# Performance work log

Measured on AMD Instinct MI355X. Metric: run time of the kernel, lower is better.

## Reference

```python
import jax, jax.numpy as jnp
import numpy as np

ACT_BIT = 8
W_BIT = 8
EPS = 1e-8


def ste_round(x):
    # straight-through round (matches torch STE quant autograd)
    return x + jax.lax.stop_gradient(jnp.round(x) - x)


def quant_act(x):
    """Per-tensor symmetric 8-bit activation quantization (HAWQ QuantAct)."""
    n = 2 ** (ACT_BIT - 1) - 1  # 127
    x_max = jax.lax.stop_gradient(jnp.max(jnp.abs(x)))
    scale = jnp.maximum(x_max, EPS) / n
    x_int = jnp.clip(ste_round(x / scale), -n - 1, n)
    return x_int * scale, scale


def quant_linear(x_q, act_scale, weight, bias):
    """Per-channel symmetric 8-bit weight quant + integer matmul + fused dequant."""
    n = 2 ** (W_BIT - 1) - 1  # 127
    w_max = jax.lax.stop_gradient(jnp.max(jnp.abs(weight), axis=1, keepdims=True))  # [out,1]
    w_scale = jnp.maximum(w_max, EPS) / n                                            # [out,1]
    w_int = jnp.clip(ste_round(weight / w_scale), -n - 1, n)                         # [out,in]
    bias_scale = w_scale[:, 0] * act_scale                                           # [out]
    b_int = ste_round(bias / bias_scale)                                             # [out]
    x_int = x_q / act_scale                                   # integer-valued float, [..., in]
    out_int = jnp.einsum('...i,oi->...o', x_int, w_int)       # int8-domain GEMM in float
    return (out_int + b_int) * bias_scale                     # fused dequant


def setup_inputs() -> dict:
    key = jax.random.key(0)
    k1, k2, k3 = jax.random.split(key, 3)
    L, B, Q, D, O = 6, 8, 1024, 1024, 1024
    hs = jax.random.normal(k1, (L, B, Q, D), dtype=jnp.float32)
    weight = jax.random.normal(k2, (O, D), dtype=jnp.float32) * 0.02
    bias = jax.random.normal(k3, (O,), dtype=jnp.float32) * 0.02
    return {"hs": hs, "weight": weight, "bias": bias}


def reference(hs, weight, bias):
    x_q, act_scale = quant_act(hs)
    return quant_linear(x_q, act_scale, weight, bias)
```

## Files before the change

kernel.cpp:

```cpp
#include <hip/hip_runtime.h>
#include <stdint.h>

typedef int i32x4 __attribute__((ext_vector_type(4)));

#define K_DIM 1024
#define BM 256
#define BN 256
#define BKK 64
#define NKT (K_DIM / BKK)


__device__ __forceinline__ int quant1(float v, float inv) {
  float t = rintf(v * inv);
  t = fminf(fmaxf(t, -128.0f), 127.0f);
  return (int)t;
}

__device__ __forceinline__ void gld_lds16(const signed char* g, signed char* l) {
  typedef const __attribute__((address_space(1))) unsigned int* gp_t;
  typedef __attribute__((address_space(3))) unsigned int* lp_t;
  __builtin_amdgcn_global_load_lds((gp_t)(const void*)g, (lp_t)(void*)l, 16, 0, 0);
}

__global__ void absmax_kernel(const float* __restrict__ x, unsigned int* __restrict__ amax,
                              long long n4) {
  long long i = (long long)blockIdx.x * blockDim.x + threadIdx.x;
  const long long stride = (long long)gridDim.x * blockDim.x;
  const float4* x4 = (const float4*)x;
  float m = 0.0f;
  for (; i < n4; i += stride) {
    float4 v = x4[i];
    m = fmaxf(m, fmaxf(fmaxf(fabsf(v.x), fabsf(v.y)), fmaxf(fabsf(v.z), fabsf(v.w))));
  }
#pragma unroll
  for (int off = 32; off > 0; off >>= 1) m = fmaxf(m, __shfl_down(m, off, 64));
  __shared__ float sm[4];
  const int lane = threadIdx.x & 63, wid = threadIdx.x >> 6;
  if (lane == 0) sm[wid] = m;
  __syncthreads();
  if (threadIdx.x == 0) {
    float b = fmaxf(fmaxf(sm[0], sm[1]), fmaxf(sm[2], sm[3]));
    atomicMax(amax, __float_as_uint(b));
  }
}

__global__ void wquant_kernel(const float* __restrict__ w, const float* __restrict__ bias,
                              const unsigned int* __restrict__ amax_u,
                              signed char* __restrict__ wq,
                              float* __restrict__ bscale, float* __restrict__ bint) {
  const int o = blockIdx.x;
  const int t = threadIdx.x;
  float4 v = ((const float4*)(w + (size_t)o * K_DIM))[t];
  float m = fmaxf(fmaxf(fabsf(v.x), fabsf(v.y)), fmaxf(fabsf(v.z), fabsf(v.w)));
#pragma unroll
  for (int off = 32; off > 0; off >>= 1) m = fmaxf(m, __shfl_down(m, off, 64));
  __shared__ float sm[4];
  __shared__ float s_scale;
  const int lane = t & 63, wid = t >> 6;
  if (lane == 0) sm[wid] = m;
  __syncthreads();
  if (t == 0) {
    float wm = fmaxf(fmaxf(sm[0], sm[1]), fmaxf(sm[2], sm[3]));
    float wsc = fmaxf(wm, 1e-8f) / 127.0f;
    float asc = fmaxf(__uint_as_float(*amax_u), 1e-8f) / 127.0f;
    float bsc = wsc * asc;
    bscale[o] = bsc;
    bint[o] = rintf(bias[o] / bsc);
    s_scale = wsc;
  }
  __syncthreads();
  const float inv = 1.0f / s_scale;
  int q0 = quant1(v.x, inv), q1 = quant1(v.y, inv), q2 = quant1(v.z, inv), q3 = quant1(v.w, inv);
  unsigned int p = (unsigned)(q0 & 255) | ((unsigned)(q1 & 255) << 8) |
                   ((unsigned)(q2 & 255) << 16) | ((unsigned)(q3 & 255) << 24);
  const int F = o >> 4, T = t >> 4;
  const int l = (((t >> 2) & 3) << 4) | (o & 15);
  const int j = (t << 2) & 15;
  *(unsigned int*)(wq + (((size_t)F << 14) + (T << 10) + (l << 4) + j)) = p;
}

__global__ void aquant_kernel(const float* __restrict__ x, const unsigned int* __restrict__ amax_u,
                              uint4* __restrict__ q16, int nchunk) {
  const float asc = fmaxf(__uint_as_float(*amax_u), 1e-8f) / 127.0f;
  const float inv = 1.0f / asc;
  int c = blockIdx.x * blockDim.x + threadIdx.x;
  const int stride = gridDim.x * blockDim.x;
  for (; c < nchunk; c += stride) {
    const int l = c & 63, T = (c >> 6) & 15, F = c >> 10;
    const size_t src = (((size_t)(F << 4) + (l & 15)) << 10) + (T << 6) + ((l >> 4) << 4);
    const float4* s4 = (const float4*)(x + src);
    unsigned int r[4];
#pragma unroll
    for (int q = 0; q < 4; q++) {
      float4 v = s4[q];
      int q0 = quant1(v.x, inv), q1 = quant1(v.y, inv), q2 = quant1(v.z, inv), q3 = quant1(v.w, inv);
      r[q] = (unsigned)(q0 & 255) | ((unsigned)(q1 & 255) << 8) |
             ((unsigned)(q2 & 255) << 16) | ((unsigned)(q3 & 255) << 24);
    }
    q16[c] = make_uint4(r[0], r[1], r[2], r[3]);
  }
}

__global__ __launch_bounds__(512, 2) void gemm_kernel(
    const signed char* __restrict__ A, const signed char* __restrict__ W,
    const float* __restrict__ bscale, const float* __restrict__ bint,
    float* __restrict__ out, int M, int N, int K) {
  extern __shared__ __align__(16) signed char smem[];
  signed char* Abase = smem;
  signed char* Bbase = smem + 65536;

  const int nwg = gridDim.x;
  const int orig = blockIdx.x;
  const int wgid = (orig & 7) * (nwg >> 3) + (orig >> 3);
  const int nbn = N / BN;
  const int bm = wgid / nbn;
  const int bn = wgid % nbn;
  const int m0 = bm * BM, n0 = bn * BN;

  const int tid = threadIdx.x;
  const int lane = tid & 63;
  const int wid = tid >> 6;
  const int wr = wid >> 2;
  const int wc = wid & 3;

  const signed char* gaf = A + (((size_t)(m0 >> 4) + wid) << 14) + (lane << 4);
  const signed char* gbf = W + (((size_t)(n0 >> 4) + wid) << 14) + (lane << 4);
  const size_t fs8 = (size_t)8 << 14;

  i32x4 acc[8][4];
#pragma unroll
  for (int i = 0; i < 8; i++)
#pragma unroll
    for (int j = 0; j < 4; j++) acc[i][j] = (i32x4){0, 0, 0, 0};

  i32x4 af[4], bf[4];

#define SB __builtin_amdgcn_sched_barrier(0)
#define BAR __builtin_amdgcn_s_barrier()
#define WAIT_LGKM0 asm volatile("s_waitcnt lgkmcnt(0)" ::: "memory")

#define ISSUE_TILE(t)                                                     \
  do {                                                                    \
    const int b_ = (t) & 3;                                               \
    const int kof_ = (t) << 10;                                           \
    gld_lds16(gaf + kof_,       Abase + ((b_ * 16 + wid) << 10));         \
    gld_lds16(gaf + fs8 + kof_, Abase + ((b_ * 16 + wid + 8) << 10));     \
    gld_lds16(gbf + kof_,       Bbase + ((b_ * 16 + wid) << 10));         \
    gld_lds16(gbf + fs8 + kof_, Bbase + ((b_ * 16 + wid + 8) << 10));     \
  } while (0)

#define RD_A(i_, mf_) af[i_] = *(const i32x4*)(Abase + (((buf_ * 16) + (mf_)) << 10) + lane * 16)
#define RD_B(j_, nf_) bf[j_] = *(const i32x4*)(Bbase + (((buf_ * 16) + (nf_)) << 10) + lane * 16)

#define MFMA8(IB, JB)                                                          \
  do {                                                                         \
    __builtin_amdgcn_s_setprio(1);                                             \
    _Pragma("unroll") for (int i_ = 0; i_ < 4; i_++)                           \
      _Pragma("unroll") for (int j_ = 0; j_ < 2; j_++)                         \
        acc[(IB) + i_][(JB) + j_] = __builtin_amdgcn_mfma_i32_16x16x64_i8(     \
            af[i_], bf[(JB) + j_], acc[(IB) + i_][(JB) + j_], 0, 0, 0);        \
    __builtin_amdgcn_s_setprio(0);                                             \
  } while (0)

#define TILE(t, DO_ISSUE, VMWAIT)                                              \
  do {                                                                         \
    const int buf_ = (t) & 3;                                                  \
                                                                  \
    RD_A(0, wr * 8 + 0); RD_A(1, wr * 8 + 1);                                  \
    RD_A(2, wr * 8 + 2); RD_A(3, wr * 8 + 3);                                  \
    RD_B(0, wc * 4 + 0); RD_B(1, wc * 4 + 1);                                  \
    if (DO_ISSUE) ISSUE_TILE((t) + 3);                                         \
    SB; BAR; SB; WAIT_LGKM0; SB;                                               \
    MFMA8(0, 0);                                                               \
    SB; BAR;                                                                   \
                                                                  \
    RD_B(2, wc * 4 + 2); RD_B(3, wc * 4 + 3);                                  \
    SB; BAR; SB; WAIT_LGKM0; SB;                                               \
    MFMA8(0, 2);                                                               \
    SB; BAR;                                                                   \
                                                                  \
    RD_A(0, wr * 8 + 4); RD_A(1, wr * 8 + 5);                                  \
    RD_A(2, wr * 8 + 6); RD_A(3, wr * 8 + 7);                                  \
    SB; BAR; SB; WAIT_LGKM0; SB;                                               \
    MFMA8(4, 2);                                                               \
    SB; BAR;                                                                   \
     \
    asm volatile("s_waitcnt " VMWAIT ::: "memory");                            \
    SB; BAR; SB;                                                               \
    MFMA8(4, 0);                                                               \
    SB; BAR;                                                                   \
  } while (0)

  ISSUE_TILE(0);
  ISSUE_TILE(1);
  ISSUE_TILE(2);
  asm volatile("s_waitcnt vmcnt(8)" ::: "memory");
  SB; BAR; SB;

#pragma unroll 1
  for (int t = 0; t < NKT - 3; ++t) {
    TILE(t, 1, "vmcnt(8)");
  }
  TILE(NKT - 3, 0, "vmcnt(4)");
  TILE(NKT - 2, 0, "vmcnt(0)");
  TILE(NKT - 1, 0, "vmcnt(0)");

#undef TILE
#undef MFMA8
#undef RD_A
#undef RD_B
#undef ISSUE_TILE

  float* Cst = (float*)smem;
  const int rr = (lane >> 4) * 4;
  const int cc = lane & 15;
#pragma unroll
  for (int h = 0; h < 2; ++h) {
    if (wr == h) {
#pragma unroll
      for (int j = 0; j < 4; j++) {
        const int colL = wc * 64 + j * 16 + cc;
        const float bs = bscale[n0 + colL];
        const float bi = bint[n0 + colL];
#pragma unroll
        for (int i = 0; i < 8; i++)
#pragma unroll
          for (int r = 0; r < 4; r++)
            Cst[(i * 16 + rr + r) * 256 + colL] = ((float)acc[i][j][r] + bi) * bs;
      }
    }
    WAIT_LGKM0;
    BAR;
    const size_t rowbase = (size_t)(m0 + h * 128) * N + n0;
#pragma unroll
    for (int it = 0; it < 16; ++it) {
      const int r_ = it * 8 + wid;
      float4 v = *(const float4*)&Cst[r_ * 256 + lane * 4];
      *(float4*)&out[rowbase + (size_t)r_ * N + lane * 4] = v;
    }
    WAIT_LGKM0;
    BAR;
  }
#undef WAIT_LGKM0
#undef BAR
#undef SB
}

extern "C" void kernel_launch(void* const* d_in, const int* in_sizes, int n_in,
                              void* d_out, int out_size, void* d_ws, size_t ws_size,
                              hipStream_t stream) {
  const float* hs = (const float*)d_in[0];
  const float* w = (const float*)d_in[1];
  const float* bias = (const float*)d_in[2];
  float* out = (float*)d_out;

  const long long n = (long long)in_sizes[0];
  const int K = K_DIM;
  const int O = in_sizes[2];
  const int M = (int)(n / K);

  char* ws = (char*)d_ws;
  unsigned int* amax_u = (unsigned int*)ws;
  float* bscale = (float*)(ws + 256);
  float* bint = (float*)(ws + 256 + 4096);
  signed char* wq = (signed char*)(ws + 65536);
  signed char* xq = (signed char*)(ws + 65536 + 1048576);

  hipFuncSetAttribute((const void*)gemm_kernel,
                      hipFuncAttributeMaxDynamicSharedMemorySize, 131072);

  hipMemsetAsync(amax_u, 0, 4, stream);

  const long long n4 = n / 4;
  absmax_kernel<<<2048, 256, 0, stream>>>(hs, amax_u, n4);
  wquant_kernel<<<O, 256, 0, stream>>>(w, bias, amax_u, wq, bscale, bint);
  const int nchunk = (int)(n / 16);
  aquant_kernel<<<2048, 256, 0, stream>>>(hs, amax_u, (uint4*)xq, nchunk);

  const int nblocks = (M / BM) * (O / BN);
  gemm_kernel<<<nblocks, 512, 131072, stream>>>(xq, wq, bscale, bint, out, M, O, K);
}
```

Baseline: 189.7 us.

## Collapse per-tile GEMM phases into a single barrier with all fragments preloaded

The int8 MFMA main loop no longer splits each K-tile into four read/compute phases separated by barriers and lgkm waits. All 8 A fragments and 4 B fragments are now loaded into registers up front, and the 32 MFMAs issue back to back, with one barrier per tile. The async global-to-LDS issue moves to the start of the tile and the final vmcnt wait is dropped. This cuts barrier and sync overhead per tile but needs more VGPRs for fragments, which could lower occupancy, and it removes the fine interleaving of LDS reads with MFMAs.

```diff
diff --git a/kernel.cpp b/kernel.cpp
--- a/kernel.cpp
+++ b/kernel.cpp
@@ -133,7 +133,7 @@
 #pragma unroll
     for (int j = 0; j < 4; j++) acc[i][j] = (i32x4){0, 0, 0, 0};
 
-  i32x4 af[4], bf[4];
+  i32x4 af[8], bf[4];
 
 #define SB __builtin_amdgcn_sched_barrier(0)
 #define BAR __builtin_amdgcn_s_barrier()
@@ -152,43 +152,30 @@
 #define RD_A(i_, mf_) af[i_] = *(const i32x4*)(Abase + (((buf_ * 16) + (mf_)) << 10) + lane * 16)
 #define RD_B(j_, nf_) bf[j_] = *(const i32x4*)(Bbase + (((buf_ * 16) + (nf_)) << 10) + lane * 16)
 
-#define MFMA8(IB, JB)                                                          \
+#define MFMA16(IB)                                                             \
   do {                                                                         \
     __builtin_amdgcn_s_setprio(1);                                             \
     _Pragma("unroll") for (int i_ = 0; i_ < 4; i_++)                           \
-      _Pragma("unroll") for (int j_ = 0; j_ < 2; j_++)                         \
-        acc[(IB) + i_][(JB) + j_] = __builtin_amdgcn_mfma_i32_16x16x64_i8(     \
-            af[i_], bf[(JB) + j_], acc[(IB) + i_][(JB) + j_], 0, 0, 0);        \
+      _Pragma("unroll") for (int j_ = 0; j_ < 4; j_++)                         \
+        acc[(IB) + i_][j_] = __builtin_amdgcn_mfma_i32_16x16x64_i8(            \
+            af[(IB) + i_], bf[j_], acc[(IB) + i_][j_], 0, 0, 0);               \
     __builtin_amdgcn_s_setprio(0);                                             \
   } while (0)
 
-#define TILE(t, DO_ISSUE, VMWAIT)                                              \
+#define TILE(t, DO_ISSUE, VMW, DO_VM)                                          \
   do {                                                                         \
     const int buf_ = (t) & 3;                                                  \
-                                                                  \
+    if (DO_ISSUE) ISSUE_TILE((t) + 3);                                         \
     RD_A(0, wr * 8 + 0); RD_A(1, wr * 8 + 1);                                  \
     RD_A(2, wr * 8 + 2); RD_A(3, wr * 8 + 3);                                  \
     RD_B(0, wc * 4 + 0); RD_B(1, wc * 4 + 1);                                  \
-    if (DO_ISSUE) ISSUE_TILE((t) + 3);                                         \
-    SB; BAR; SB; WAIT_LGKM0; SB;                                               \
-    MFMA8(0, 0);                                                               \
-    SB; BAR;                                                                   \
-                                                                  \
     RD_B(2, wc * 4 + 2); RD_B(3, wc * 4 + 3);                                  \
-    SB; BAR; SB; WAIT_LGKM0; SB;                                               \
-    MFMA8(0, 2);                                                               \
-    SB; BAR;                                                                   \
-                                                                  \
-    RD_A(0, wr * 8 + 4); RD_A(1, wr * 8 + 5);                                  \
-    RD_A(2, wr * 8 + 6); RD_A(3, wr * 8 + 7);                                  \
-    SB; BAR; SB; WAIT_LGKM0; SB;                                               \
-    MFMA8(4, 2);                                                               \
-    SB; BAR;                                                                   \
-     \
-    asm volatile("s_waitcnt " VMWAIT ::: "memory");                            \
+    RD_A(4, wr * 8 + 4); RD_A(5, wr * 8 + 5);                                  \
+    RD_A(6, wr * 8 + 6); RD_A(7, wr * 8 + 7);                                  \
+    MFMA16(0);                                                                 \
+    MFMA16(4);                                                                 \
+    if (DO_VM) { asm volatile("s_waitcnt " VMW ::: "memory"); }                \
     SB; BAR; SB;                                                               \
-    MFMA8(4, 0);                                                               \
-    SB; BAR;                                                                   \
   } while (0)
 
   ISSUE_TILE(0);
@@ -199,14 +186,14 @@
 
 #pragma unroll 1
   for (int t = 0; t < NKT - 3; ++t) {
-    TILE(t, 1, "vmcnt(8)");
-  }
-  TILE(NKT - 3, 0, "vmcnt(4)");
-  TILE(NKT - 2, 0, "vmcnt(0)");
-  TILE(NKT - 1, 0, "vmcnt(0)");
+    TILE(t, 1, "vmcnt(8)", 1);
+  }
+  TILE(NKT - 3, 0, "vmcnt(4)", 1);
+  TILE(NKT - 2, 0, "vmcnt(0)", 1);
+  TILE(NKT - 1, 0, "", 0);
 
 #undef TILE
-#undef MFMA8
+#undef MFMA16
 #undef RD_A
 #undef RD_B
 #undef ISSUE_TILE
```

Measured after the change: 186.4 us. No clear change (-1.7%).
